# Kernel tuning notes

Measured on AMD Instinct MI355X. Metric: run time of the kernel, lower is better.

Reference implementation:

```python
import jax, jax.numpy as jnp
import numpy as np

OUT, IN = 4096, 4096
GROUP_SIZE = 128
NUMEL = OUT * IN                 # 16,777,216 int4 values
N_GROUPS = NUMEL // GROUP_SIZE   # 131,072
N_PACKED = NUMEL // 2            # 8,388,608 bytes (stored as int32 0..255)


def _dequantize_int4(q_packed, q_scales, q_zeros):
    """Unpack two 4-bit values per byte, dequant per group, reshape to (OUT, IN)."""
    low = q_packed & 0xF                     # [N_PACKED]
    high = (q_packed >> 4) & 0xF             # [N_PACKED]
    # interleave: flat[2i] = low nibble, flat[2i+1] = high nibble
    q = jnp.stack([low, high], axis=-1).reshape(NUMEL)            # [NUMEL] int
    qg = q.astype(jnp.float32).reshape(N_GROUPS, GROUP_SIZE)      # [G, group]
    w = (qg - q_zeros[:, None]) * q_scales[:, None]
    return w.reshape(OUT, IN)


def setup_inputs() -> dict:
    key = jax.random.key(0)
    k = jax.random.split(key, 6)
    x = jax.random.normal(k[0], (4, 2048, IN), dtype=jnp.float32)
    q_packed = jax.random.randint(k[1], (N_PACKED,), 0, 256, dtype=jnp.int32)
    q_scales = jax.random.uniform(k[2], (N_GROUPS,), dtype=jnp.float32) * 0.02 + 1e-3
    q_zeros = jax.random.uniform(k[3], (N_GROUPS,), dtype=jnp.float32) * 15.0
    delta_weight = jax.random.normal(k[4], (OUT, IN), dtype=jnp.float32) * 0.01
    bias = jax.random.normal(k[5], (OUT,), dtype=jnp.float32)
    return {"x": x, "q_packed": q_packed, "q_scales": q_scales,
            "q_zeros": q_zeros, "delta_weight": delta_weight, "bias": bias}


def reference(x, q_packed, q_scales, q_zeros, delta_weight, bias):
    W = _dequantize_int4(q_packed, q_scales, q_zeros)   # [OUT, IN]
    W_eff = W + delta_weight
    # F.linear: y = x @ W_eff^T + bias
    h = jnp.einsum('bsi,oi->bso', x, W_eff) + bias
    return h
```

## Files before the change

### kernel.cpp

```cpp
#include <hip/hip_runtime.h>


#define M_DIM 8192
#define N_DIM 4096
#define K_DIM 4096
#define NUMEL (N_DIM * K_DIM)

typedef _Float16 half_t;
typedef __attribute__((ext_vector_type(4))) _Float16 half4v;
typedef __attribute__((ext_vector_type(8))) _Float16 half8v;
typedef __attribute__((ext_vector_type(8))) short short8v;
typedef __attribute__((ext_vector_type(8))) unsigned short ushort8v;
typedef __attribute__((ext_vector_type(4))) float float4v;
typedef __attribute__((ext_vector_type(4))) int int4v;

#define KTILES 64
#define LDT 72

static __device__ __forceinline__ void gload16(const void* g, void* l) {
    __builtin_amdgcn_global_load_lds(
        (const __attribute__((address_space(1))) void*)g,
        (__attribute__((address_space(3))) void*)l, 16, 0, 0);
}

static __device__ __forceinline__ unsigned short f2bf(float f) {
    unsigned u = __builtin_bit_cast(unsigned, f);
    u += 0x7fffu + ((u >> 16) & 1u);
    return (unsigned short)(u >> 16);
}

__global__ __launch_bounds__(256) void k_pack_w(
    const int* __restrict__ qp, const float* __restrict__ sc,
    const float* __restrict__ zr, const float* __restrict__ dwt,
    unsigned char* __restrict__ Wp)
{
    const size_t o = ((size_t)blockIdx.x * 256 + threadIdx.x) << 4;
    const int chunk16 = (int)(o >> 14);
    const int c  = (int)(o >> 10) & 15;
    const int ln = (int)(o >> 4) & 63;
    const int n = (chunk16 >> 6) * 128 + (c >> 1) * 16 + (ln & 15);
    const int k = (chunk16 & 63) * 64 + (c & 1) * 32 + (ln >> 4) * 8;
    const long flat = (long)n * K_DIM + k;
    const int g = n * 32 + (k >> 7);
    const float s = sc[g];
    const float zs = zr[g] * s;
    int4v q4 = *(const int4v*)(qp + (flat >> 1));
    float4v d0 = *(const float4v*)(dwt + flat);
    float4v d1 = *(const float4v*)(dwt + flat + 4);
    float d[8] = {d0[0], d0[1], d0[2], d0[3], d1[0], d1[1], d1[2], d1[3]};
    ushort8v vh;
#pragma unroll
    for (int j = 0; j < 4; ++j) {
        vh[2*j]   = f2bf(fmaf((float)(q4[j] & 15),        s, d[2*j]   - zs));
        vh[2*j+1] = f2bf(fmaf((float)((q4[j] >> 4) & 15), s, d[2*j+1] - zs));
    }
    *(ushort8v*)(Wp + o) = vh;
}

__global__ __launch_bounds__(256) void k_pack_x(
    const float* __restrict__ X, unsigned char* __restrict__ Xp)
{
    const size_t o = ((size_t)blockIdx.x * 256 + threadIdx.x) << 4;
    const int chunk16 = (int)(o >> 14);
    const int c  = (int)(o >> 10) & 15;
    const int ln = (int)(o >> 4) & 63;
    const int m = (chunk16 >> 6) * 128 + (c >> 1) * 16 + (ln & 15);
    const int k = (chunk16 & 63) * 64 + (c & 1) * 32 + (ln >> 4) * 8;
    const float* src = X + (size_t)m * K_DIM + k;
    float4v x0 = *(const float4v*)(src);
    float4v x1 = *(const float4v*)(src + 4);
    ushort8v vh;
    vh[0] = f2bf(x0[0]); vh[1] = f2bf(x0[1]);
    vh[2] = f2bf(x0[2]); vh[3] = f2bf(x0[3]);
    vh[4] = f2bf(x1[0]); vh[5] = f2bf(x1[1]);
    vh[6] = f2bf(x1[2]); vh[7] = f2bf(x1[3]);
    *(ushort8v*)(Xp + o) = vh;
}

#define BARX() do { __builtin_amdgcn_sched_barrier(0); \
                    __builtin_amdgcn_s_barrier(); \
                    __builtin_amdgcn_sched_barrier(0); } while(0)
#define WAITV_(N) do { __builtin_amdgcn_sched_barrier(0); \
                       asm volatile("s_waitcnt vmcnt(" #N ")" ::: "memory"); \
                       __builtin_amdgcn_sched_barrier(0); } while(0)
#define WAITV(N) WAITV_(N)

#define STAGE_A(BUF, T) do { \
    const unsigned char* s0_ = ap0 + ((size_t)(T) << 14); \
    const unsigned char* s1_ = ap1 + ((size_t)(T) << 14); \
    gload16(s0_,        &lds4[BUF][t16]); \
    gload16(s0_ + 8192, &lds4[BUF][t16 + 8192]); \
    gload16(s1_,        &lds4[BUF][16384 + t16]); \
    gload16(s1_ + 8192, &lds4[BUF][16384 + t16 + 8192]); \
} while(0)

#define LOADB01(SET, T) do { \
_Pragma("unroll") for (int j_ = 0; j_ < 2; ++j_) \
_Pragma("unroll") for (int ks_ = 0; ks_ < 2; ++ks_) \
        SET[j_][ks_] = *(const short8v*)(bgl + ((size_t)(T) << 14) \
                                             + ((j_ * 2 + ks_) << 10)); \
} while(0)

#define LOADB23(T) do { \
_Pragma("unroll") for (int j_ = 0; j_ < 2; ++j_) \
_Pragma("unroll") for (int ks_ = 0; ks_ < 2; ++ks_) \
        b23[j_][ks_] = *(const short8v*)(bgl + ((size_t)(T) << 14) \
                                             + (((2 + j_) * 2 + ks_) << 10)); \
} while(0)

#define READ_A(BUF, F0) do { \
_Pragma("unroll") for (int i_ = 0; i_ < 4; ++i_) \
_Pragma("unroll") for (int ks_ = 0; ks_ < 2; ++ks_) \
        ah[i_][ks_] = *(const short8v*)(&lds4[BUF] \
            [awm + ((((F0) + i_) * 2 + ks_) << 10) + lane16]); \
} while(0)

#define MFMA_Q(F0, N0, BREG) do { \
    __builtin_amdgcn_s_setprio(1); \
_Pragma("unroll") for (int i_ = 0; i_ < 4; ++i_) \
_Pragma("unroll") for (int j_ = 0; j_ < 2; ++j_) \
_Pragma("unroll") for (int ks_ = 0; ks_ < 2; ++ks_) \
        acc[(F0)+i_][(N0)+j_] = __builtin_amdgcn_mfma_f32_16x16x32_bf16( \
            ah[i_][ks_], BREG[j_][ks_], acc[(F0)+i_][(N0)+j_], 0, 0, 0); \
    __builtin_amdgcn_s_setprio(0); \
} while(0)

#define BODY(RBUF, SBUF, BCUR, BNXT, T, STG, LDB, WVN) do { \
    if (STG) { STAGE_A(SBUF, (T) + 2); } \
    __builtin_amdgcn_sched_barrier(0); \
    if (LDB) { LOADB01(BNXT, (T) + 1); } \
    READ_A(RBUF, 0); \
    MFMA_Q(0, 0, BCUR); \
    MFMA_Q(0, 2, b23); \
    READ_A(RBUF, 4); \
    MFMA_Q(4, 2, b23); \
    if (LDB) { LOADB23((T) + 1); } \
    MFMA_Q(4, 0, BCUR); \
    WAITV(WVN); \
    BARX(); \
} while(0)

__global__ __launch_bounds__(512, 2) void k_gemm_breg(
    const unsigned char* __restrict__ Apk, const unsigned char* __restrict__ Bpk,
    const float* __restrict__ bias, float* __restrict__ Y)
{
    __shared__ __align__(16) unsigned char lds4[4][32768];

    const int tid  = threadIdx.x;
    const int lane = tid & 63;
    const int wave = tid >> 6;
    const int wm = wave >> 2;
    const int wn = wave & 3;
    const int lane16 = lane << 4;
    const int t16 = tid << 4;
    const int awm = wm << 14;

    const int wg = blockIdx.x;
    const int swg = (wg & 7) * 64 + (wg >> 3);
    const int bn = swg & 15;
    const int bm = swg >> 4;

    const unsigned char* ap0 = Apk + (((size_t)(2 * bm)     * KTILES) << 14) + t16;
    const unsigned char* ap1 = Apk + (((size_t)(2 * bm + 1) * KTILES) << 14) + t16;
    const unsigned char* bgl = Bpk + (((size_t)(2 * bn + (wn >> 1)) * KTILES) << 14)
                             + ((wn & 1) << 13) + lane16;

    short8v ah[4][2], b01A[2][2], b01B[2][2], b23[2][2];
    float4v acc[8][4];
    const float4v zero4 = {0.f, 0.f, 0.f, 0.f};
#pragma unroll
    for (int i = 0; i < 8; ++i)
#pragma unroll
        for (int j = 0; j < 4; ++j) acc[i][j] = zero4;

    STAGE_A(0, 0);
    STAGE_A(1, 1);
    __builtin_amdgcn_sched_barrier(0);
    LOADB01(b01A, 0);
    LOADB23(0);
    WAITV(12);
    BARX();

    for (int it = 0; it < 15; ++it) {
        const int t0 = it << 2;
        BODY(0, 2, b01A, b01B, t0,     1, 1, 20);
        BODY(1, 3, b01B, b01A, t0 + 1, 1, 1, 20);
        BODY(2, 0, b01A, b01B, t0 + 2, 1, 1, 20);
        BODY(3, 1, b01B, b01A, t0 + 3, 1, 1, 20);
    }
    BODY(0, 2, b01A, b01B, 60, 1, 1, 20);
    BODY(1, 3, b01B, b01A, 61, 1, 1, 20);
    BODY(2, 0, b01A, b01B, 62, 0, 1, 8);
    READ_A(3, 0);
    MFMA_Q(0, 0, b01B);
    MFMA_Q(0, 2, b23);
    READ_A(3, 4);
    MFMA_Q(4, 2, b23);
    MFMA_Q(4, 0, b01B);

    const long m0 = (long)bm * 256 + wm * 128;
    const long n0 = (long)bn * 256 + wn * 64;
#pragma unroll
    for (int mf = 0; mf < 8; ++mf) {
        const long row = m0 + mf * 16 + (lane >> 4) * 4;
#pragma unroll
        for (int nf = 0; nf < 4; ++nf) {
            const long col = n0 + nf * 16 + (lane & 15);
            const float b = bias[col];
#pragma unroll
            for (int r = 0; r < 4; ++r)
                Y[(row + r) * N_DIM + col] = acc[mf][nf][r] + b;
        }
    }
}

__global__ __launch_bounds__(256, 2) void k_gemm_fused(
    const float* __restrict__ X, const int* __restrict__ qp,
    const float* __restrict__ sc, const float* __restrict__ zr,
    const float* __restrict__ dwt,
    const float* __restrict__ bias, float* __restrict__ Y)
{
    __shared__ __align__(16) half_t Ah[128 * LDT];
    __shared__ __align__(16) half_t Bh[128 * LDT];

    const int tid  = threadIdx.x;
    const int lane = tid & 63;
    const int wave = tid >> 6;
    const int wm = wave >> 1, wn = wave & 1;
    const int bn = blockIdx.x & 31;
    const int bm = blockIdx.x >> 5;
    const long m0 = (long)bm * 128;
    const long n0 = (long)bn * 128;
    const int fr = lane & 15;
    const int ko = (lane >> 4) * 8;

    const float4v zero4 = {0.f, 0.f, 0.f, 0.f};
    float4v acc[4][4];
#pragma unroll
    for (int i = 0; i < 4; ++i)
#pragma unroll
        for (int j = 0; j < 4; ++j) acc[i][j] = zero4;

    for (int k0 = 0; k0 < K_DIM; k0 += 64) {
        {
            const int ar = tid >> 4;
            const int ac = (tid & 15) * 4;
#pragma unroll
            for (int rr = 0; rr < 8; ++rr) {
                const int row = ar + rr * 16;
                float4v xv = *(const float4v*)(X + (m0 + row) * K_DIM + k0 + ac);
                half4v h;
#pragma unroll
                for (int j = 0; j < 4; ++j) h[j] = (half_t)xv[j];
                *(half4v*)(Ah + row * LDT + ac) = h;
            }
        }
        {
            const int cr = tid >> 3;
            const int cc = (tid & 7) * 8;
#pragma unroll
            for (int rr = 0; rr < 4; ++rr) {
                const int row = cr + rr * 32;
                const long n = n0 + row;
                const int g = (int)(n * 32 + (k0 >> 7));
                const float s = sc[g];
                const float zs = zr[g] * s;
                const long flat = n * K_DIM + k0 + cc;
                int4v q4 = *(const int4v*)(qp + (flat >> 1));
                float4v d0 = *(const float4v*)(dwt + flat);
                float4v d1 = *(const float4v*)(dwt + flat + 4);
                float d[8] = {d0[0], d0[1], d0[2], d0[3], d1[0], d1[1], d1[2], d1[3]};
                half8v vh;
#pragma unroll
                for (int j = 0; j < 4; ++j) {
                    vh[2*j]   = (half_t)fmaf((float)(q4[j] & 15),        s, d[2*j]   - zs);
                    vh[2*j+1] = (half_t)fmaf((float)((q4[j] >> 4) & 15), s, d[2*j+1] - zs);
                }
                *(half8v*)(Bh + row * LDT + cc) = vh;
            }
        }
        __syncthreads();
#pragma unroll
        for (int ks = 0; ks < 2; ++ks) {
            const int kk = ks * 32 + ko;
            half8v a2[4], b2[4];
#pragma unroll
            for (int i = 0; i < 4; ++i) {
                a2[i] = *(const half8v*)(Ah + (wm * 64 + i * 16 + fr) * LDT + kk);
                b2[i] = *(const half8v*)(Bh + (wn * 64 + i * 16 + fr) * LDT + kk);
            }
#pragma unroll
            for (int i = 0; i < 4; ++i)
#pragma unroll
                for (int j = 0; j < 4; ++j)
                    acc[i][j] = __builtin_amdgcn_mfma_f32_16x16x32_f16(
                        a2[i], b2[j], acc[i][j], 0, 0, 0);
        }
        __syncthreads();
    }

#pragma unroll
    for (int i = 0; i < 4; ++i) {
        const long mrow = m0 + wm * 64 + i * 16 + (lane >> 4) * 4;
#pragma unroll
        for (int j = 0; j < 4; ++j) {
            const long col = n0 + wn * 64 + j * 16 + (lane & 15);
            const float b = bias[col];
#pragma unroll
            for (int r = 0; r < 4; ++r)
                Y[(mrow + r) * N_DIM + col] = acc[i][j][r] + b;
        }
    }
}

extern "C" void kernel_launch(void* const* d_in, const int* in_sizes, int n_in,
                              void* d_out, int out_size, void* d_ws, size_t ws_size,
                              hipStream_t stream)
{
    const float* X  = (const float*)d_in[0];
    const int*   qp = (const int*)d_in[1];
    const float* sc = (const float*)d_in[2];
    const float* zr = (const float*)d_in[3];
    const float* dwt = (const float*)d_in[4];
    const float* bs = (const float*)d_in[5];
    float* Y = (float*)d_out;

    const size_t needB = (size_t)N_DIM * K_DIM * 2;
    const size_t needA = (size_t)M_DIM * K_DIM * 2;

    if (ws_size >= needA + needB) {
        unsigned char* Bpk = (unsigned char*)d_ws;
        unsigned char* Apk = Bpk + needB;
        k_pack_w<<<dim3((unsigned)(needB >> 12)), dim3(256), 0, stream>>>(qp, sc, zr, dwt, Bpk);
        k_pack_x<<<dim3((unsigned)(needA >> 12)), dim3(256), 0, stream>>>(X, Apk);
        k_gemm_breg<<<dim3((M_DIM / 256) * (N_DIM / 256)), dim3(512), 0, stream>>>(Apk, Bpk, bs, Y);
    } else {
        k_gemm_fused<<<dim3((M_DIM / 128) * (N_DIM / 128)), dim3(256), 0, stream>>>(
            X, qp, sc, zr, dwt, bs, Y);
    }
}
```

Before: 286.1 us.

## Stage both A and B tiles through LDS with 32-wide K steps

The GEMM used to stream B fragments from global memory straight into registers and staged only A in LDS, in 64-wide K tiles. Now A and B both go through LDS by async global-to-LDS loads in 32-wide K sub-tiles, so the pipeline has twice as many iterations with one barrier each. This frees the registers that held double-buffered B and lets the 4 waves that share a B slice reuse it from LDS instead of each loading it. In exchange there are more barriers per K and more LDS read traffic.

```diff
diff --git a/kernel.cpp b/kernel.cpp
--- a/kernel.cpp
+++ b/kernel.cpp
@@ -80,67 +80,48 @@
 #define BARX() do { __builtin_amdgcn_sched_barrier(0); \
                     __builtin_amdgcn_s_barrier(); \
                     __builtin_amdgcn_sched_barrier(0); } while(0)
-#define WAITV_(N) do { __builtin_amdgcn_sched_barrier(0); \
-                       asm volatile("s_waitcnt vmcnt(" #N ")" ::: "memory"); \
-                       __builtin_amdgcn_sched_barrier(0); } while(0)
-#define WAITV(N) WAITV_(N)
-
-#define STAGE_A(BUF, T) do { \
-    const unsigned char* s0_ = ap0 + ((size_t)(T) << 14); \
-    const unsigned char* s1_ = ap1 + ((size_t)(T) << 14); \
-    gload16(s0_,        &lds4[BUF][t16]); \
-    gload16(s0_ + 8192, &lds4[BUF][t16 + 8192]); \
-    gload16(s1_,        &lds4[BUF][16384 + t16]); \
-    gload16(s1_ + 8192, &lds4[BUF][16384 + t16 + 8192]); \
-} while(0)
-
-#define LOADB01(SET, T) do { \
-_Pragma("unroll") for (int j_ = 0; j_ < 2; ++j_) \
-_Pragma("unroll") for (int ks_ = 0; ks_ < 2; ++ks_) \
-        SET[j_][ks_] = *(const short8v*)(bgl + ((size_t)(T) << 14) \
-                                             + ((j_ * 2 + ks_) << 10)); \
-} while(0)
-
-#define LOADB23(T) do { \
-_Pragma("unroll") for (int j_ = 0; j_ < 2; ++j_) \
-_Pragma("unroll") for (int ks_ = 0; ks_ < 2; ++ks_) \
-        b23[j_][ks_] = *(const short8v*)(bgl + ((size_t)(T) << 14) \
-                                             + (((2 + j_) * 2 + ks_) << 10)); \
-} while(0)
-
-#define READ_A(BUF, F0) do { \
+#define WAITV(N) do { __builtin_amdgcn_sched_barrier(0); \
+                      asm volatile("s_waitcnt vmcnt(" #N ")" ::: "memory"); \
+                      __builtin_amdgcn_sched_barrier(0); } while(0)
+
+#define STAGE32(BUF, T) do { \
+    const size_t ko_ = ((size_t)((T) >> 1) << 14) + (size_t)(((T) & 1) << 10) + soff; \
+    gload16(a0s + ko_, &lds4[BUF][t16]); \
+    gload16(a1s + ko_, &lds4[BUF][8192 + t16]); \
+    gload16(b0s + ko_, &lds4[BUF][16384 + t16]); \
+    gload16(b1s + ko_, &lds4[BUF][24576 + t16]); \
+} while(0)
+
+#define RD_A4(BUF, I0) do { \
 _Pragma("unroll") for (int i_ = 0; i_ < 4; ++i_) \
-_Pragma("unroll") for (int ks_ = 0; ks_ < 2; ++ks_) \
-        ah[i_][ks_] = *(const short8v*)(&lds4[BUF] \
-            [awm + ((((F0) + i_) * 2 + ks_) << 10) + lane16]); \
-} while(0)
-
-#define MFMA_Q(F0, N0, BREG) do { \
+        af[i_] = *(const short8v*)(&lds4[BUF][aoff + (((I0) + i_) << 10)]); \
+} while(0)
+
+#define RD_B4(BUF) do { \
+_Pragma("unroll") for (int j_ = 0; j_ < 4; ++j_) \
+        bf[j_] = *(const short8v*)(&lds4[BUF][boff + (j_ << 10)]); \
+} while(0)
+
+#define MF16(A0) do { \
     __builtin_amdgcn_s_setprio(1); \
 _Pragma("unroll") for (int i_ = 0; i_ < 4; ++i_) \
-_Pragma("unroll") for (int j_ = 0; j_ < 2; ++j_) \
-_Pragma("unroll") for (int ks_ = 0; ks_ < 2; ++ks_) \
-        acc[(F0)+i_][(N0)+j_] = __builtin_amdgcn_mfma_f32_16x16x32_bf16( \
-            ah[i_][ks_], BREG[j_][ks_], acc[(F0)+i_][(N0)+j_], 0, 0, 0); \
+_Pragma("unroll") for (int j_ = 0; j_ < 4; ++j_) \
+        acc[(A0)+i_][j_] = __builtin_amdgcn_mfma_f32_16x16x32_bf16( \
+            af[i_], bf[j_], acc[(A0)+i_][j_], 0, 0, 0); \
     __builtin_amdgcn_s_setprio(0); \
 } while(0)
 
-#define BODY(RBUF, SBUF, BCUR, BNXT, T, STG, LDB, WVN) do { \
-    if (STG) { STAGE_A(SBUF, (T) + 2); } \
-    __builtin_amdgcn_sched_barrier(0); \
-    if (LDB) { LOADB01(BNXT, (T) + 1); } \
-    READ_A(RBUF, 0); \
-    MFMA_Q(0, 0, BCUR); \
-    MFMA_Q(0, 2, b23); \
-    READ_A(RBUF, 4); \
-    MFMA_Q(4, 2, b23); \
-    if (LDB) { LOADB23((T) + 1); } \
-    MFMA_Q(4, 0, BCUR); \
+#define BODY(RB, SB, T, STG, WVN) do { \
+    if (STG) { STAGE32(SB, (T) + 2); } \
     WAITV(WVN); \
     BARX(); \
-} while(0)
-
-__global__ __launch_bounds__(512, 2) void k_gemm_breg(
+    RD_A4(RB, 0); RD_B4(RB); \
+    MF16(0); \
+    RD_A4(RB, 4); \
+    MF16(4); \
+} while(0)
+
+__global__ __launch_bounds__(512, 2) void k_gemm_b32(
     const unsigned char* __restrict__ Apk, const unsigned char* __restrict__ Bpk,
     const float* __restrict__ bias, float* __restrict__ Y)
 {
@@ -153,19 +134,21 @@
     const int wn = wave & 3;
     const int lane16 = lane << 4;
     const int t16 = tid << 4;
-    const int awm = wm << 14;
+    const int aoff = (wm << 13) + lane16;
+    const int boff = 16384 + ((wn >> 1) << 13) + ((wn & 1) << 12) + lane16;
 
     const int wg = blockIdx.x;
     const int swg = (wg & 7) * 64 + (wg >> 3);
     const int bn = swg & 15;
     const int bm = swg >> 4;
 
-    const unsigned char* ap0 = Apk + (((size_t)(2 * bm)     * KTILES) << 14) + t16;
-    const unsigned char* ap1 = Apk + (((size_t)(2 * bm + 1) * KTILES) << 14) + t16;
-    const unsigned char* bgl = Bpk + (((size_t)(2 * bn + (wn >> 1)) * KTILES) << 14)
-                             + ((wn & 1) << 13) + lane16;
-
-    short8v ah[4][2], b01A[2][2], b01B[2][2], b23[2][2];
+    const size_t soff = ((size_t)(tid >> 6) << 11) + (size_t)((tid & 63) << 4);
+    const unsigned char* a0s = Apk + (((size_t)(2 * bm)     * KTILES) << 14);
+    const unsigned char* a1s = Apk + (((size_t)(2 * bm + 1) * KTILES) << 14);
+    const unsigned char* b0s = Bpk + (((size_t)(2 * bn)     * KTILES) << 14);
+    const unsigned char* b1s = Bpk + (((size_t)(2 * bn + 1) * KTILES) << 14);
+
+    short8v af[4], bf[4];
     float4v acc[8][4];
     const float4v zero4 = {0.f, 0.f, 0.f, 0.f};
 #pragma unroll
@@ -173,30 +156,21 @@
 #pragma unroll
         for (int j = 0; j < 4; ++j) acc[i][j] = zero4;
 
-    STAGE_A(0, 0);
-    STAGE_A(1, 1);
-    __builtin_amdgcn_sched_barrier(0);
-    LOADB01(b01A, 0);
-    LOADB23(0);
-    WAITV(12);
-    BARX();
-
-    for (int it = 0; it < 15; ++it) {
+    STAGE32(0, 0);
+    STAGE32(1, 1);
+    WAITV(4);
+
+    for (int it = 0; it < 31; ++it) {
         const int t0 = it << 2;
-        BODY(0, 2, b01A, b01B, t0,     1, 1, 20);
-        BODY(1, 3, b01B, b01A, t0 + 1, 1, 1, 20);
-        BODY(2, 0, b01A, b01B, t0 + 2, 1, 1, 20);
-        BODY(3, 1, b01B, b01A, t0 + 3, 1, 1, 20);
-    }
-    BODY(0, 2, b01A, b01B, 60, 1, 1, 20);
-    BODY(1, 3, b01B, b01A, 61, 1, 1, 20);
-    BODY(2, 0, b01A, b01B, 62, 0, 1, 8);
-    READ_A(3, 0);
-    MFMA_Q(0, 0, b01B);
-    MFMA_Q(0, 2, b23);
-    READ_A(3, 4);
-    MFMA_Q(4, 2, b23);
-    MFMA_Q(4, 0, b01B);
+        BODY(0, 2, t0,     1, 8);
+        BODY(1, 3, t0 + 1, 1, 8);
+        BODY(2, 0, t0 + 2, 1, 8);
+        BODY(3, 1, t0 + 3, 1, 8);
+    }
+    BODY(0, 2, 124, 1, 8);
+    BODY(1, 3, 125, 1, 8);
+    BODY(2, 0, 126, 0, 4);
+    BODY(3, 0, 127, 0, 0);
 
     const long m0 = (long)bm * 256 + wm * 128;
     const long n0 = (long)bn * 256 + wn * 64;
@@ -333,7 +307,7 @@
         unsigned char* Apk = Bpk + needB;
         k_pack_w<<<dim3((unsigned)(needB >> 12)), dim3(256), 0, stream>>>(qp, sc, zr, dwt, Bpk);
         k_pack_x<<<dim3((unsigned)(needA >> 12)), dim3(256), 0, stream>>>(X, Apk);
-        k_gemm_breg<<<dim3((M_DIM / 256) * (N_DIM / 256)), dim3(512), 0, stream>>>(Apk, Bpk, bs, Y);
+        k_gemm_b32<<<dim3((M_DIM / 256) * (N_DIM / 256)), dim3(512), 0, stream>>>(Apk, Bpk, bs, Y);
     } else {
         k_gemm_fused<<<dim3((M_DIM / 128) * (N_DIM / 128)), dim3(256), 0, stream>>>(
             X, qp, sc, zr, dwt, bs, Y);
```

Result: faster. 280.0 us (-2.1%).
